# Optimization experiments

Hardware: AMD Instinct MI355X
Metric: run time of the kernel (lower is better)

## Reference

```python
import jax, jax.numpy as jnp
import numpy as np

B, T, C_IN, H, W = 128, 12, 10, 25, 25
HID = 64
DN = ('NCHW', 'OIHW', 'NCHW')


def setup_inputs() -> dict:
    key = jax.random.key(0)
    ks = jax.random.split(key, 8)
    x = jax.random.normal(ks[0], (B, T, C_IN, H, W), dtype=jnp.float32)
    # ConvLSTM cell: conv over concat([x, h]) -> 4*HID gate channels, 3x3 kernel
    conv_w = jax.random.normal(ks[1], (4 * HID, C_IN + HID, 3, 3), dtype=jnp.float32) * 0.05
    conv_b = jnp.zeros((4 * HID,), dtype=jnp.float32)
    # MLP head: hidden*25*25 -> 16 -> 8 -> 2
    w1 = jax.random.normal(ks[2], (HID * H * W, 16), dtype=jnp.float32) * 0.01
    b1 = jnp.zeros((16,), dtype=jnp.float32)
    w2 = jax.random.normal(ks[3], (16, 8), dtype=jnp.float32) * 0.1
    b2 = jnp.zeros((8,), dtype=jnp.float32)
    w3 = jax.random.normal(ks[4], (8, 2), dtype=jnp.float32) * 0.1
    b3 = jnp.zeros((2,), dtype=jnp.float32)
    return {"x": x, "conv_w": conv_w, "conv_b": conv_b,
            "w1": w1, "b1": b1, "w2": w2, "b2": b2, "w3": w3, "b3": b3}


def _convlstm_last_h(x, conv_w, conv_b):
    # x: (B,T,C,H,W); returns last hidden state h_T: (B,HID,H,W)
    h0 = jnp.zeros((x.shape[0], HID, H, W), dtype=x.dtype)
    c0 = jnp.zeros_like(h0)

    def step(carry, xt):
        h, c = carry
        inp = jnp.concatenate([xt, h], axis=1)              # (B, C+HID, H, W)
        gates = jax.lax.conv_general_dilated(
            inp, conv_w, window_strides=(1, 1), padding='SAME',
            dimension_numbers=DN) + conv_b[None, :, None, None]  # (B,4*HID,H,W)
        i, f, o, g = jnp.split(gates, 4, axis=1)
        i, f, o = jax.nn.sigmoid(i), jax.nn.sigmoid(f), jax.nn.sigmoid(o)
        g = jnp.tanh(g)
        c_new = f * c + i * g
        h_new = o * jnp.tanh(c_new)
        return (h_new, c_new), None

    (h_last, _), _ = jax.lax.scan(step, (h0, c0), jnp.swapaxes(x, 0, 1))
    return h_last


def reference(x, conv_w, conv_b, w1, b1, w2, b2, w3, b3):
    h = _convlstm_last_h(x, conv_w, conv_b)          # (B,HID,25,25)
    h = jax.nn.relu(h).reshape(h.shape[0], -1)       # flatten
    # dropout is identity in eval mode
    h = jax.nn.relu(h @ w1 + b1)
    h = jax.nn.relu(h @ w2 + b2)
    logits = h @ w3 + b3                             # (B,2)
    return jax.nn.log_softmax(logits, axis=1)
```

## Files before the change

kernel.cpp:

```cpp
#include <hip/hip_runtime.h>
#include <hip/hip_bf16.h>
#include <math.h>

#define BATCH 128
#define TT    12
#define CIN   10
#define HID   64
#define PLANE 625
#define NU    10
#define IPB   50000
#define NKB   45
#define CSZ   (BATCH*PLANE*HID)

typedef __attribute__((ext_vector_type(8)))  short bf16x8;
typedef __attribute__((ext_vector_type(16))) float f32x16;

__device__ __forceinline__ float fsigm(float v){ return 1.f/(1.f+__expf(-v)); }
__device__ __forceinline__ float ftanh(float v){ return 1.f - 2.f/(__expf(2.f*v)+1.f); }
__device__ __forceinline__ unsigned short f2bf(float v){
    __hip_bfloat16 b = __float2bfloat16(v);
    return *reinterpret_cast<unsigned short*>(&b);
}

__global__ void k_wprep(const float* __restrict__ w, unsigned short* __restrict__ wpk){
    int tid = blockIdx.x*256 + threadIdx.x;
    if (tid >= NKB*8*64) return;
    int lane = tid & 63;
    int nt   = (tid >> 6) & 7;
    int kb   = tid >> 9;
    int tap = kb/5, ci = kb - tap*5;
    int ky = tap/3, kx = tap - ky*3;
    int g = lane & 3, jlo = (lane & 31) >> 2, kh = lane >> 5;
    int o = g*64 + nt*8 + jlo;
    union { unsigned short u[8]; float4 f; } pk;
    #pragma unroll
    for (int e = 0; e < 8; ++e){
        int ch = ci*16 + kh*8 + e;
        float v = (ch < 74) ? w[((o*74 + ch)*3 + ky)*3 + kx] : 0.f;
        pk.u[e] = f2bf(v);
    }
    *reinterpret_cast<float4*>(wpk + (size_t)tid*8) = pk.f;
}

__global__ void k_xcopy(const float* __restrict__ x, unsigned short* __restrict__ inp, int t){
    int idx = blockIdx.x*256 + threadIdx.x;
    if (idx >= BATCH*CIN*PLANE) return;
    int m  = idx % PLANE;
    int r  = idx / PLANE;
    int ch = r % CIN;
    int b  = r / CIN;
    float v = x[((size_t)(b*TT + t)*CIN + ch)*PLANE + m];
    inp[(size_t)b*IPB + ((((ch>>3)*PLANE) + m)<<3) + (ch&7)] = f2bf(v);
}

__global__ __launch_bounds__(512) void k_gemm(
    const float* __restrict__ x,
    const unsigned short* __restrict__ inp,
    unsigned short* __restrict__ inpn,
    const unsigned short* __restrict__ wpk,
    const float* __restrict__ bias,
    float* __restrict__ cbuf,
    float* __restrict__ hbuf,
    int t)
{
    __shared__ __align__(16) unsigned short at2[2160*8];

    const int tid  = threadIdx.x;
    const int mg   = blockIdx.x;
    const int b    = blockIdx.y;
    const int lane = tid & 63;
    const int nt   = tid >> 6;
    const int r0row = (mg*128)/25;

    const unsigned short* ib = inp + (size_t)b*IPB;
    for (int idx = tid; idx < 2160; idx += 512){
        int q   = idx/216, pix = idx - q*216;
        int rr  = pix/27,  cc  = pix - rr*27;
        int gr  = r0row - 1 + rr, gc = cc - 1;
        float4 v = {0.f,0.f,0.f,0.f};
        if ((unsigned)gr < 25u && (unsigned)gc < 25u)
            v = *reinterpret_cast<const float4*>(ib + (((size_t)q*PLANE + gr*25 + gc)<<3));
        *reinterpret_cast<float4*>(at2 + ((size_t)idx<<3)) = v;
    }

    const int kh = lane >> 5;
    const unsigned short* ap[4];
    #pragma unroll
    for (int mt = 0; mt < 4; ++mt){
        int m = mg*128 + mt*32 + (lane & 31);
        int row = m/25, col = m - row*25;
        int pm = (row - r0row + 1)*27 + col;
        ap[mt] = at2 + ((kh*216 + pm - 27) << 3);
    }

    f32x16 acc[4];
    #pragma unroll
    for (int mt = 0; mt < 4; ++mt)
        #pragma unroll
        for (int e = 0; e < 16; ++e) acc[mt][e] = 0.f;

    __syncthreads();

    const bf16x8* wptr = reinterpret_cast<const bf16x8*>(wpk) + nt*64 + lane;
    bf16x8 bcur = *wptr;
    const unsigned short *a0 = ap[0], *a1 = ap[1], *a2 = ap[2], *a3 = ap[3];
    #pragma unroll 1
    for (int tap = 0; tap < 9; ++tap){
        #pragma unroll
        for (int ci = 0; ci < 5; ++ci){
            bf16x8 bnxt = wptr[512];
            wptr += 512;
            bf16x8 f0 = *reinterpret_cast<const bf16x8*>(a0 + ci*3456);
            bf16x8 f1 = *reinterpret_cast<const bf16x8*>(a1 + ci*3456);
            bf16x8 f2 = *reinterpret_cast<const bf16x8*>(a2 + ci*3456);
            bf16x8 f3 = *reinterpret_cast<const bf16x8*>(a3 + ci*3456);
            acc[0] = __builtin_amdgcn_mfma_f32_32x32x16_bf16(f0, bcur, acc[0], 0,0,0);
            acc[1] = __builtin_amdgcn_mfma_f32_32x32x16_bf16(f1, bcur, acc[1], 0,0,0);
            acc[2] = __builtin_amdgcn_mfma_f32_32x32x16_bf16(f2, bcur, acc[2], 0,0,0);
            acc[3] = __builtin_amdgcn_mfma_f32_32x32x16_bf16(f3, bcur, acc[3], 0,0,0);
            bcur = bnxt;
        }
        const int d = (tap == 2 || tap == 5) ? 25*8 : 8;
        a0 += d; a1 += d; a2 += d; a3 += d;
    }

    const int g   = lane & 3;
    const int jlo = (lane & 31) >> 2;
    const int j   = nt*8 + jlo;
    const float bown = bias[g*64 + j];
    const float sA = (g == 3) ? 2.f : 1.f;
    const float sB = (g == 3) ? -1.f : 0.f;
    const int  mbase = mg*128 + 4*kh;
    const bool gb0 = (g & 1), gb1 = (g & 2);
    float* cb = cbuf + (size_t)b*PLANE*HID;
    float* hb = hbuf + (size_t)b*PLANE*HID;
    unsigned short* hn = inpn + (size_t)b*IPB;
    const int chh = CIN + j, uh = chh >> 3, sh = chh & 7;

    #pragma unroll
    for (int mt = 0; mt < 4; ++mt){
        #pragma unroll
        for (int rq = 0; rq < 4; ++rq){
            float v0 = fmaf(sA, fsigm(sA*(acc[mt][rq*4+0] + bown)), sB);
            float v1 = fmaf(sA, fsigm(sA*(acc[mt][rq*4+1] + bown)), sB);
            float v2 = fmaf(sA, fsigm(sA*(acc[mt][rq*4+2] + bown)), sB);
            float v3 = fmaf(sA, fsigm(sA*(acc[mt][rq*4+3] + bown)), sB);
            float s;
            s = __shfl_xor(gb0 ? v0 : v1, 1); if (gb0) v0 = s; else v1 = s;
            s = __shfl_xor(gb0 ? v2 : v3, 1); if (gb0) v2 = s; else v3 = s;
            s = __shfl_xor(gb1 ? v0 : v2, 2); if (gb1) v0 = s; else v2 = s;
            s = __shfl_xor(gb1 ? v1 : v3, 2); if (gb1) v1 = s; else v3 = s;
            const int m = mbase + mt*32 + g + 8*rq;
            if (m < PLANE){
                float co = cb[m*HID + j];
                float cn = fmaf(v1, co, v0*v3);
                float h  = v2 * ftanh(cn);
                cb[m*HID + j] = cn;
                hn[((uh*PLANE + m) << 3) + sh] = f2bf(h);
                if (t == TT-1) hb[m*HID + j] = h;
            }
        }
    }

    if (t < TT-1){
        const float* xn = x + (size_t)(b*TT + t + 1)*CIN*PLANE;
        for (int idx = tid; idx < 1280; idx += 512){
            int ch = idx >> 7, mi = idx & 127;
            int m = mg*128 + mi;
            if (m < PLANE)
                inpn[(size_t)b*IPB + ((((ch>>3)*PLANE) + m)<<3) + (ch&7)] =
                    f2bf(xn[ch*PLANE + m]);
        }
    }
}

__global__ __launch_bounds__(256) void k_mlp(
    const float* __restrict__ hfin,
    const float* __restrict__ w1, const float* __restrict__ b1,
    const float* __restrict__ w2, const float* __restrict__ b2,
    const float* __restrict__ w3, const float* __restrict__ b3,
    float* __restrict__ out)
{
    __shared__ float red[256][17];
    __shared__ float hid1[16];
    __shared__ float hid2[8];
    const int b = blockIdx.x, tid = threadIdx.x;

    float acc[16];
    #pragma unroll
    for (int i = 0; i < 16; ++i) acc[i] = 0.f;

    const float* hbb = hfin + (size_t)b * (HID * PLANE);
    for (int kidx = tid; kidx < HID * PLANE; kidx += 256){
        int m = kidx >> 6, j = kidx & 63;
        float hv = hbb[kidx];
        hv = hv > 0.f ? hv : 0.f;
        const float* wf = w1 + (size_t)(j*PLANE + m) * 16;
        #pragma unroll
        for (int i = 0; i < 16; ++i) acc[i] = fmaf(hv, wf[i], acc[i]);
    }
    #pragma unroll
    for (int i = 0; i < 16; ++i) red[tid][i] = acc[i];
    __syncthreads();

    if (tid < 16){
        float s = b1[tid];
        for (int t2 = 0; t2 < 256; ++t2) s += red[t2][tid];
        hid1[tid] = s > 0.f ? s : 0.f;
    }
    __syncthreads();
    if (tid < 8){
        float s = b2[tid];
        #pragma unroll
        for (int k2 = 0; k2 < 16; ++k2) s += hid1[k2] * w2[k2*8 + tid];
        hid2[tid] = s > 0.f ? s : 0.f;
    }
    __syncthreads();
    if (tid == 0){
        float l0 = b3[0], l1 = b3[1];
        #pragma unroll
        for (int k3 = 0; k3 < 8; ++k3){ l0 += hid2[k3]*w3[k3*2]; l1 += hid2[k3]*w3[k3*2+1]; }
        float m   = fmaxf(l0, l1);
        float lse = m + logf(__expf(l0 - m) + __expf(l1 - m));
        out[b*2 + 0] = l0 - lse;
        out[b*2 + 1] = l1 - lse;
    }
}

extern "C" void kernel_launch(void* const* d_in, const int* in_sizes, int n_in,
                              void* d_out, int out_size, void* d_ws, size_t ws_size,
                              hipStream_t stream) {
    const float* x      = (const float*)d_in[0];
    const float* conv_w = (const float*)d_in[1];
    const float* conv_b = (const float*)d_in[2];
    const float* w1     = (const float*)d_in[3];
    const float* b1     = (const float*)d_in[4];
    const float* w2     = (const float*)d_in[5];
    const float* b2     = (const float*)d_in[6];
    const float* w3     = (const float*)d_in[7];
    const float* b3     = (const float*)d_in[8];
    float* out = (float*)d_out;

    unsigned short* inp0 = (unsigned short*)d_ws;
    unsigned short* inp1 = inp0 + (size_t)BATCH*IPB;
    float* c   = (float*)(inp1 + (size_t)BATCH*IPB);
    float* hb  = c + CSZ;
    unsigned short* wpk = (unsigned short*)(hb + CSZ);

    hipMemsetAsync(inp0, 0, (size_t)BATCH*IPB*2, stream);
    hipMemsetAsync(inp1, 0, (size_t)BATCH*IPB*2, stream);
    hipMemsetAsync(c,    0, (size_t)CSZ*4,       stream);

    k_wprep<<<dim3(90),   dim3(256), 0, stream>>>(conv_w, wpk);
    k_xcopy<<<dim3(3125), dim3(256), 0, stream>>>(x, inp0, 0);

    for (int t = 0; t < TT; ++t){
        unsigned short* ic  = (t & 1) ? inp1 : inp0;
        unsigned short* in_ = (t & 1) ? inp0 : inp1;
        k_gemm<<<dim3(5, BATCH), dim3(512), 0, stream>>>(x, ic, in_, wpk, conv_b, c, hb, t);
    }
    k_mlp<<<dim3(BATCH), dim3(256), 0, stream>>>(hb, w1, b1, w2, b2, w3, b3, out);
}
```

Before: 726.8 us.

## Split MLP first layer across K chunks with coalesced weight reads

Replaces the one-block-per-sample MLP with a split-K kernel (10 chunks per sample, 1280 blocks) that walks w1 in its natural row order using float4 loads and reduces with wavefront shuffles. A second tiny kernel sums the partials and runs the small layers and log-softmax. The aim is to raise parallelism and make the 2.5 MB w1 reads contiguous instead of strided, at the cost of an extra launch and a strided gather from h.

```diff
diff --git a/kernel.cpp b/kernel.cpp
--- a/kernel.cpp
+++ b/kernel.cpp
@@ -11,6 +11,7 @@
 #define IPB   50000
 #define NKB   45
 #define CSZ   (BATCH*PLANE*HID)
+#define KSPLIT 10
 
 typedef __attribute__((ext_vector_type(8)))  short bf16x8;
 typedef __attribute__((ext_vector_type(16))) float f32x16;
@@ -174,57 +175,79 @@
     }
 }
 
-__global__ __launch_bounds__(256) void k_mlp(
-    const float* __restrict__ hfin,
-    const float* __restrict__ w1, const float* __restrict__ b1,
+__global__ __launch_bounds__(256) void k_mlp1(
+    const float* __restrict__ hfin, const float* __restrict__ w1,
+    float* __restrict__ part)
+{
+    __shared__ float xw[4][16];
+    const int ks = blockIdx.x, b = blockIdx.y, tid = threadIdx.x;
+    const float* hbb = hfin + (size_t)b * (HID * PLANE);
+
+    float acc[16];
+    #pragma unroll
+    for (int i = 0; i < 16; ++i) acc[i] = 0.f;
+
+    const int kw0 = ks * 4000, kw1 = kw0 + 4000;
+    for (int kw = kw0 + tid; kw < kw1; kw += 256){
+        int j = kw / 625, m = kw - j * 625;
+        float hv = hbb[m * 64 + j];
+        hv = hv > 0.f ? hv : 0.f;
+        const float4* wf = (const float4*)(w1 + (size_t)kw * 16);
+        float4 wa = wf[0], wb = wf[1], wc = wf[2], wd = wf[3];
+        acc[ 0] = fmaf(hv, wa.x, acc[ 0]); acc[ 1] = fmaf(hv, wa.y, acc[ 1]);
+        acc[ 2] = fmaf(hv, wa.z, acc[ 2]); acc[ 3] = fmaf(hv, wa.w, acc[ 3]);
+        acc[ 4] = fmaf(hv, wb.x, acc[ 4]); acc[ 5] = fmaf(hv, wb.y, acc[ 5]);
+        acc[ 6] = fmaf(hv, wb.z, acc[ 6]); acc[ 7] = fmaf(hv, wb.w, acc[ 7]);
+        acc[ 8] = fmaf(hv, wc.x, acc[ 8]); acc[ 9] = fmaf(hv, wc.y, acc[ 9]);
+        acc[10] = fmaf(hv, wc.z, acc[10]); acc[11] = fmaf(hv, wc.w, acc[11]);
+        acc[12] = fmaf(hv, wd.x, acc[12]); acc[13] = fmaf(hv, wd.y, acc[13]);
+        acc[14] = fmaf(hv, wd.z, acc[14]); acc[15] = fmaf(hv, wd.w, acc[15]);
+    }
+    #pragma unroll
+    for (int d = 1; d < 64; d <<= 1)
+        #pragma unroll
+        for (int i = 0; i < 16; ++i) acc[i] += __shfl_xor(acc[i], d);
+    if ((tid & 63) == 0)
+        #pragma unroll
+        for (int i = 0; i < 16; ++i) xw[tid >> 6][i] = acc[i];
+    __syncthreads();
+    if (tid < 16)
+        part[((size_t)b * KSPLIT + ks) * 16 + tid] =
+            xw[0][tid] + xw[1][tid] + xw[2][tid] + xw[3][tid];
+}
+
+__global__ __launch_bounds__(128) void k_mlp2(
+    const float* __restrict__ part,
+    const float* __restrict__ b1,
     const float* __restrict__ w2, const float* __restrict__ b2,
     const float* __restrict__ w3, const float* __restrict__ b3,
     float* __restrict__ out)
 {
-    __shared__ float red[256][17];
-    __shared__ float hid1[16];
-    __shared__ float hid2[8];
-    const int b = blockIdx.x, tid = threadIdx.x;
-
-    float acc[16];
-    #pragma unroll
-    for (int i = 0; i < 16; ++i) acc[i] = 0.f;
-
-    const float* hbb = hfin + (size_t)b * (HID * PLANE);
-    for (int kidx = tid; kidx < HID * PLANE; kidx += 256){
-        int m = kidx >> 6, j = kidx & 63;
-        float hv = hbb[kidx];
-        hv = hv > 0.f ? hv : 0.f;
-        const float* wf = w1 + (size_t)(j*PLANE + m) * 16;
-        #pragma unroll
-        for (int i = 0; i < 16; ++i) acc[i] = fmaf(hv, wf[i], acc[i]);
-    }
-    #pragma unroll
-    for (int i = 0; i < 16; ++i) red[tid][i] = acc[i];
-    __syncthreads();
-
-    if (tid < 16){
-        float s = b1[tid];
-        for (int t2 = 0; t2 < 256; ++t2) s += red[t2][tid];
-        hid1[tid] = s > 0.f ? s : 0.f;
-    }
-    __syncthreads();
-    if (tid < 8){
-        float s = b2[tid];
-        #pragma unroll
-        for (int k2 = 0; k2 < 16; ++k2) s += hid1[k2] * w2[k2*8 + tid];
-        hid2[tid] = s > 0.f ? s : 0.f;
-    }
-    __syncthreads();
-    if (tid == 0){
-        float l0 = b3[0], l1 = b3[1];
-        #pragma unroll
-        for (int k3 = 0; k3 < 8; ++k3){ l0 += hid2[k3]*w3[k3*2]; l1 += hid2[k3]*w3[k3*2+1]; }
-        float m   = fmaxf(l0, l1);
-        float lse = m + logf(__expf(l0 - m) + __expf(l1 - m));
-        out[b*2 + 0] = l0 - lse;
-        out[b*2 + 1] = l1 - lse;
-    }
+    const int b = threadIdx.x;
+    float h1[16];
+    #pragma unroll
+    for (int i = 0; i < 16; ++i) h1[i] = b1[i];
+    for (int s = 0; s < KSPLIT; ++s)
+        #pragma unroll
+        for (int i = 0; i < 16; ++i) h1[i] += part[((size_t)b * KSPLIT + s) * 16 + i];
+    #pragma unroll
+    for (int i = 0; i < 16; ++i) h1[i] = h1[i] > 0.f ? h1[i] : 0.f;
+
+    float h2[8];
+    #pragma unroll
+    for (int i = 0; i < 8; ++i){
+        float s2 = b2[i];
+        #pragma unroll
+        for (int k2 = 0; k2 < 16; ++k2) s2 += h1[k2] * w2[k2*8 + i];
+        h2[i] = s2 > 0.f ? s2 : 0.f;
+    }
+    float l0 = b3[0], l1 = b3[1];
+    #pragma unroll
+    for (int k3 = 0; k3 < 8; ++k3){ l0 += h2[k3]*w3[k3*2]; l1 += h2[k3]*w3[k3*2+1]; }
+    float m   = fmaxf(l0, l1);
+    float lse = m + logf(__expf(l0 - m) + __expf(l1 - m));
+    out[b*2 + 0] = l0 - lse;
+    out[b*2 + 1] = l1 - lse;
 }
 
 extern "C" void kernel_launch(void* const* d_in, const int* in_sizes, int n_in,
@@ -246,6 +269,7 @@
     float* c   = (float*)(inp1 + (size_t)BATCH*IPB);
     float* hb  = c + CSZ;
     unsigned short* wpk = (unsigned short*)(hb + CSZ);
+    float* part = (float*)(wpk + (size_t)(NKB+1)*8*64*8);
 
     hipMemsetAsync(inp0, 0, (size_t)BATCH*IPB*2, stream);
     hipMemsetAsync(inp1, 0, (size_t)BATCH*IPB*2, stream);
@@ -259,5 +283,6 @@
         unsigned short* in_ = (t & 1) ? inp0 : inp1;
         k_gemm<<<dim3(5, BATCH), dim3(512), 0, stream>>>(x, ic, in_, wpk, conv_b, c, hb, t);
     }
-    k_mlp<<<dim3(BATCH), dim3(256), 0, stream>>>(hb, w1, b1, w2, b2, w3, b3, out);
-}
+    k_mlp1<<<dim3(KSPLIT, BATCH), dim3(256), 0, stream>>>(hb, w1, part);
+    k_mlp2<<<dim3(1), dim3(128), 0, stream>>>(part, b1, w2, b2, w3, b3, out);
+}
```

After: 732.9 us. About the same (+0.8%).
